# Kernel optimization log

Hardware: AMD Instinct MI355X
Metric: run time of the kernel (lower is better)

Reference implementation:

```python
import jax, jax.numpy as jnp
import numpy as np

B, D, C = 512, 512, 85742   # batch, in_features, out_features (MS1M identities)
M = 4                       # angular margin order -> cos(4*theta) = 8c^4 - 8c^2 + 1
PI = 3.14159265             # constant used in the torch source
LAMB = max(5.0, 1000.0 * (1.0 + 0.12 * 1) ** -1.0)  # lamb at iter=1 (first forward)
EPS = 1e-12                 # torch F.normalize eps


def setup_inputs() -> dict:
    key = jax.random.key(0)
    k1, k2, k3 = jax.random.split(key, 3)
    x = jax.random.normal(k1, (B, D), dtype=jnp.float32)
    label = jax.random.randint(k2, (B,), 0, C)
    limit = np.sqrt(6.0 / (D + C))  # xavier_uniform bound for weight [C, D]
    weight = jax.random.uniform(k3, (C, D), minval=-limit, maxval=limit, dtype=jnp.float32)
    return {"x": x, "weight": weight, "label": label}


def reference(x, weight, label):
    # row-normalize features and class weights (F.normalize, p=2, dim=1)
    xn = x / jnp.maximum(jnp.linalg.norm(x, axis=1, keepdims=True), EPS)
    wn = weight / jnp.maximum(jnp.linalg.norm(weight, axis=1, keepdims=True), EPS)
    cos = jnp.clip(xn @ wn.T, -1.0, 1.0)                       # [B, C] cosine logits
    cos_m = 8.0 * cos**4 - 8.0 * cos**2 + 1.0                  # cos(4*theta), m=4
    # theta/k computed on detached cos (torch uses cos_theta.data)
    theta = jnp.arccos(jax.lax.stop_gradient(cos))
    k = jnp.floor(M * theta / PI)
    phi = (-1.0) ** k * cos_m - 2.0 * k                        # [B, C]
    feat_norm = jnp.linalg.norm(x, axis=1)                     # [B]
    one_hot = jax.nn.one_hot(label, C, dtype=cos.dtype)        # scatter of 1s at label
    out = (one_hot * (phi - cos) / (1.0 + LAMB) + cos) * feat_norm[:, None]
    # cross-entropy, mean reduction
    logp = jax.nn.log_softmax(out, axis=1)
    loss = -jnp.take_along_axis(logp, label[:, None], axis=1).mean()
    return loss
```

## Files before the change

### kernel.cpp

```cpp
#include <hip/hip_runtime.h>
#include <stdint.h>

#define D_K 512
#define B_ROWS 512
#define C_CLS 85742
#define N_TILES 670
#define N_PART (N_TILES * 2)

using bf16x8 = __attribute__((ext_vector_type(8))) short;
using f32x4  = __attribute__((ext_vector_type(4))) float;

__device__ __forceinline__ unsigned short f2bf(float f) {
  unsigned int u = __builtin_bit_cast(unsigned int, f);
  u += 0x7FFFu + ((u >> 16) & 1u);
  return (unsigned short)(u >> 16);
}
__device__ __forceinline__ float bf2f(unsigned short h) {
  return __builtin_bit_cast(float, ((unsigned int)h) << 16);
}
__device__ __forceinline__ float sq8(const float4& a, const float4& b) {
  return a.x*a.x + a.y*a.y + a.z*a.z + a.w*a.w +
         b.x*b.x + b.y*b.y + b.z*b.z + b.w*b.w;
}
__device__ __forceinline__ void pack8(const float4& a, const float4& b, unsigned short* h) {
  h[0]=f2bf(a.x); h[1]=f2bf(a.y); h[2]=f2bf(a.z); h[3]=f2bf(a.w);
  h[4]=f2bf(b.x); h[5]=f2bf(b.y); h[6]=f2bf(b.z); h[7]=f2bf(b.w);
}

__global__ __launch_bounds__(256) void k_xnorm(const float* __restrict__ X,
                                               unsigned short* __restrict__ XN,
                                               float* __restrict__ FN) {
  int row  = blockIdx.x * 4 + (threadIdx.x >> 6);
  int lane = threadIdx.x & 63;
  const float4* px = (const float4*)(X + (size_t)row * D_K + lane * 8);
  float4 u = px[0], v = px[1];
  float nsq = sq8(u, v);
#pragma unroll
  for (int m = 1; m <= 32; m <<= 1) nsq += __shfl_xor(nsq, m);
  float nrm = sqrtf(nsq);
  float inv = 1.0f / fmaxf(nrm, 1e-12f);
  float4 a = make_float4(u.x*inv, u.y*inv, u.z*inv, u.w*inv);
  float4 b = make_float4(v.x*inv, v.y*inv, v.z*inv, v.w*inv);
  alignas(16) unsigned short h[8];
  pack8(a, b, h);
  *(bf16x8*)(XN + (size_t)row * D_K + lane * 8) = *(const bf16x8*)h;
  if (lane == 0) FN[row] = nrm;
}

__global__ __launch_bounds__(256) void k_gemm_lse(const float* __restrict__ W,
                                                  const unsigned short* __restrict__ XN,
                                                  const float* __restrict__ FN,
                                                  float2* __restrict__ PART) {
  __shared__ alignas(16) unsigned short As[128 * 32];
  __shared__ alignas(16) unsigned short Bs[128 * 32];
  __shared__ float nsqS[128];
  __shared__ float fnS[128];

  int bid = blockIdx.x;
  int wg    = (bid & 7) * 335 + (bid >> 3);
  int ntile = wg >> 2, mtile = wg & 3;
  int m0 = mtile * 128, n0 = ntile * 128;

  int t    = threadIdx.x;
  int lane = t & 63, wid = t >> 6;
  int wm = wid >> 1, wn = wid & 1;
  int s = lane & 15, g = lane >> 4;

  int r1 = t >> 2;
  int c0 = (t & 3) * 8;
  int gr1 = n0 + r1, gr2 = n0 + 64 + r1;
  bool v1 = gr1 < C_CLS, v2 = gr2 < C_CLS;
  const float* pB1 = W + (size_t)gr1 * D_K + c0;
  const float* pB2 = W + (size_t)gr2 * D_K + c0;

  int lin0 = wid * 512 + lane * 8;
  int lin1 = 2048 + lin0;
  const unsigned short* gA0 = XN + (size_t)(m0 + (lin0 >> 5)) * D_K + (lin0 & 31);
  const unsigned short* gA1 = XN + (size_t)(m0 + (lin1 >> 5)) * D_K + (lin1 & 31);
  unsigned short* ldsA0 = As + wid * 512;
  unsigned short* ldsA1 = As + 2048 + wid * 512;

  f32x4 acc[4][4] = {};
  float nsq1 = 0.f, nsq2 = 0.f;

  float4 ra0, ra1, rb0, rb1;
  float4 z4 = make_float4(0.f, 0.f, 0.f, 0.f);
  if (v1) { ra0 = *(const float4*)pB1; ra1 = *(const float4*)(pB1 + 4); } else { ra0 = z4; ra1 = z4; }
  if (v2) { rb0 = *(const float4*)pB2; rb1 = *(const float4*)(pB2 + 4); } else { rb0 = z4; rb1 = z4; }

  for (int kt = 0; kt < 16; ++kt) {
    __syncthreads();
    nsq1 += sq8(ra0, ra1);
    nsq2 += sq8(rb0, rb1);
    alignas(16) unsigned short h1[8], h2[8];
    pack8(ra0, ra1, h1);
    pack8(rb0, rb1, h2);
    *(bf16x8*)(Bs + t * 8)        = *(const bf16x8*)h1;
    *(bf16x8*)(Bs + 2048 + t * 8) = *(const bf16x8*)h2;
    __builtin_amdgcn_global_load_lds(
        (const __attribute__((address_space(1))) unsigned int*)(gA0 + kt * 32),
        (__attribute__((address_space(3))) unsigned int*)ldsA0, 16, 0, 0);
    __builtin_amdgcn_global_load_lds(
        (const __attribute__((address_space(1))) unsigned int*)(gA1 + kt * 32),
        (__attribute__((address_space(3))) unsigned int*)ldsA1, 16, 0, 0);
    __syncthreads();
    if (kt + 1 < 16) {
      const float* q1 = pB1 + (kt + 1) * 32;
      const float* q2 = pB2 + (kt + 1) * 32;
      if (v1) { ra0 = *(const float4*)q1; ra1 = *(const float4*)(q1 + 4); }
      if (v2) { rb0 = *(const float4*)q2; rb1 = *(const float4*)(q2 + 4); }
    }
    bf16x8 af[4], bfr[4];
#pragma unroll
    for (int mf = 0; mf < 4; ++mf)
      af[mf] = *(const bf16x8*)(As + (wm * 64 + mf * 16 + s) * 32 + g * 8);
#pragma unroll
    for (int nf = 0; nf < 4; ++nf)
      bfr[nf] = *(const bf16x8*)(Bs + (wn * 64 + nf * 16 + s) * 32 + g * 8);
#pragma unroll
    for (int mf = 0; mf < 4; ++mf)
#pragma unroll
      for (int nf = 0; nf < 4; ++nf)
        acc[mf][nf] = __builtin_amdgcn_mfma_f32_16x16x32_bf16(af[mf], bfr[nf], acc[mf][nf], 0, 0, 0);
  }

  nsq1 += __shfl_xor(nsq1, 1); nsq1 += __shfl_xor(nsq1, 2);
  nsq2 += __shfl_xor(nsq2, 1); nsq2 += __shfl_xor(nsq2, 2);
  if ((t & 3) == 0) { nsqS[r1] = nsq1; nsqS[64 + r1] = nsq2; }
  if (t < 128) fnS[t] = FN[m0 + t];
  __syncthreads();

  float rinv[4]; int cvalid[4];
#pragma unroll
  for (int nf = 0; nf < 4; ++nf) {
    int cl = wn * 64 + nf * 16 + s;
    cvalid[nf] = (n0 + cl) < C_CLS;
    rinv[nf] = 1.0f / fmaxf(sqrtf(nsqS[cl]), 1e-12f);
  }
  const float NEG_INF = -__builtin_inff();
#pragma unroll
  for (int mf = 0; mf < 4; ++mf) {
#pragma unroll
    for (int q = 0; q < 4; ++q) {
      int rl = wm * 64 + mf * 16 + g * 4 + q;
      float fr = fnS[rl];
      float z[4]; float mx = NEG_INF;
#pragma unroll
      for (int nf = 0; nf < 4; ++nf) {
        float cc = acc[mf][nf][q] * rinv[nf];
        cc = fminf(fmaxf(cc, -1.0f), 1.0f);
        z[nf] = cvalid[nf] ? cc * fr : NEG_INF;
        mx = fmaxf(mx, z[nf]);
      }
#pragma unroll
      for (int d = 1; d <= 8; d <<= 1) mx = fmaxf(mx, __shfl_xor(mx, d));
      float se = 0.f;
#pragma unroll
      for (int nf = 0; nf < 4; ++nf) se += __expf(z[nf] - mx);
#pragma unroll
      for (int d = 1; d <= 8; d <<= 1) se += __shfl_xor(se, d);
      if (s == mf * 4 + q)
        PART[(size_t)(m0 + rl) * N_PART + (ntile * 2 + wn)] = make_float2(mx, se);
    }
  }
}

__global__ __launch_bounds__(64) void k_target(const float* __restrict__ W,
                                               const unsigned short* __restrict__ XN,
                                               const float* __restrict__ FN,
                                               const int* __restrict__ LBL,
                                               float2* __restrict__ ZT) {
  int row = blockIdx.x;
  int lane = threadIdx.x;
  int lab = LBL[row];
  const float* pw = W + (size_t)lab * D_K + lane * 8;
  const unsigned short* px = XN + (size_t)row * D_K + lane * 8;
  float dot = 0.f, nsq = 0.f;
#pragma unroll
  for (int j = 0; j < 8; ++j) {
    float w = pw[j];
    nsq += w * w;
    dot += bf2f(px[j]) * bf2f(f2bf(w));
  }
#pragma unroll
  for (int m = 1; m <= 32; m <<= 1) { dot += __shfl_xor(dot, m); nsq += __shfl_xor(nsq, m); }
  if (lane == 0) {
    const float LAMB = 1000.0f / 1.12f;
    float rinv = 1.0f / fmaxf(sqrtf(nsq), 1e-12f);
    float c = fminf(fmaxf(dot * rinv, -1.0f), 1.0f);
    float c2 = c * c;
    float cm = 8.0f * c2 * c2 - 8.0f * c2 + 1.0f;
    float th = acosf(c);
    float kf = floorf(4.0f * th / 3.14159265f);
    float phi = ((((int)kf) & 1) ? -cm : cm) - 2.0f * kf;
    float fr = FN[row];
    float zu = fr * c;
    float zm = fr * (c + (phi - c) / (1.0f + LAMB));
    ZT[row] = make_float2(zu, zm);
  }
}

__global__ __launch_bounds__(256) void k_lse(const float2* __restrict__ PART,
                                             const float2* __restrict__ ZT,
                                             float* __restrict__ LOSSI) {
  int row = blockIdx.x;
  int t = threadIdx.x;
  const float NEG_INF = -__builtin_inff();
  float m = NEG_INF, ss = 0.f;
  for (int p = t; p < N_PART; p += 256) {
    float2 ps = PART[(size_t)row * N_PART + p];
    if (ps.y > 0.f) {
      if (ps.x > m) { ss = ss * __expf(m - ps.x) + ps.y; m = ps.x; }
      else          { ss += ps.y * __expf(ps.x - m); }
    }
  }
  __shared__ float sm[256], sv[256];
  sm[t] = m; sv[t] = ss;
  __syncthreads();
  for (int o = 128; o > 0; o >>= 1) {
    if (t < o) {
      float m1 = sm[t], s1 = sv[t];
      float m2 = sm[t + o], s2 = sv[t + o];
      float mm = fmaxf(m1, m2);
      float e1 = (m1 > NEG_INF) ? s1 * __expf(m1 - mm) : 0.f;
      float e2 = (m2 > NEG_INF) ? s2 * __expf(m2 - mm) : 0.f;
      sm[t] = mm; sv[t] = e1 + e2;
    }
    __syncthreads();
  }
  if (t == 0) {
    float M = sm[0], S = sv[0];
    float2 zt = ZT[row];
    S += __expf(zt.y - M) - __expf(zt.x - M);
    LOSSI[row] = M + logf(S) - zt.y;
  }
}

__global__ __launch_bounds__(256) void k_mean(const float* __restrict__ LOSSI,
                                              float* __restrict__ OUT) {
  int t = threadIdx.x;
  float s_ = LOSSI[t] + LOSSI[t + 256];
#pragma unroll
  for (int m = 1; m <= 32; m <<= 1) s_ += __shfl_xor(s_, m);
  __shared__ float wsum[4];
  if ((t & 63) == 0) wsum[t >> 6] = s_;
  __syncthreads();
  if (t == 0) OUT[0] = (wsum[0] + wsum[1] + wsum[2] + wsum[3]) * (1.0f / 512.0f);
}

extern "C" void kernel_launch(void* const* d_in, const int* in_sizes, int n_in,
                              void* d_out, int out_size, void* d_ws, size_t ws_size,
                              hipStream_t stream) {
  const float* X   = (const float*)d_in[0];
  const float* W   = (const float*)d_in[1];
  const int*   LBL = (const int*)d_in[2];
  float* OUT = (float*)d_out;

  char* ws = (char*)d_ws;
  unsigned short* XN = (unsigned short*)ws;
  float*  FN    = (float*)(ws + 524288);
  float2* ZT    = (float2*)(ws + 526336);
  float*  LOSSI = (float*)(ws + 530432);
  float2* PART  = (float2*)(ws + 532480);

  k_xnorm  <<<dim3(128),  dim3(256), 0, stream>>>(X, XN, FN);
  k_gemm_lse<<<dim3(2680), dim3(256), 0, stream>>>(W, XN, FN, PART);
  k_target <<<dim3(512),  dim3(64),  0, stream>>>(W, XN, FN, LBL, ZT);
  k_lse    <<<dim3(512),  dim3(256), 0, stream>>>(PART, ZT, LOSSI);
  k_mean   <<<dim3(1),    dim3(256), 0, stream>>>(LOSSI, OUT);
}
```

Baseline: 111.7 us.

## Double-buffer LDS tiles in GEMM with explicit waitcnt barriers

Restructures the GEMM main loop to ping-pong between two LDS buffers for both the X (bf16, loaded with async global-to-LDS copies) and W tiles. Compute on one buffer now overlaps staging of the next, and each k-step needs only one barrier with a partial vmcnt wait instead of two full syncthreads. The W load mapping also changes: each thread loads 16 contiguous floats of one row, with clamped row indices instead of zero-fill branches. The cost is double the LDS footprint and reliance on hand-written waitcnt counts matching the number of outstanding loads.

Result: slower. 145.7 us (+30.4%).

```diff
diff --git a/kernel.cpp b/kernel.cpp
--- a/kernel.cpp
+++ b/kernel.cpp
@@ -2,7 +2,6 @@
 #include <stdint.h>
 
 #define D_K 512
-#define B_ROWS 512
 #define C_CLS 85742
 #define N_TILES 670
 #define N_PART (N_TILES * 2)
@@ -51,8 +50,8 @@
                                                   const unsigned short* __restrict__ XN,
                                                   const float* __restrict__ FN,
                                                   float2* __restrict__ PART) {
-  __shared__ alignas(16) unsigned short As[128 * 32];
-  __shared__ alignas(16) unsigned short Bs[128 * 32];
+  __shared__ alignas(16) unsigned short As[2][4096];
+  __shared__ alignas(16) unsigned short Bs[2][4096];
   __shared__ float nsqS[128];
   __shared__ float fnS[128];
 
@@ -66,67 +65,87 @@
   int wm = wid >> 1, wn = wid & 1;
   int s = lane & 15, g = lane >> 4;
 
-  int r1 = t >> 2;
-  int c0 = (t & 3) * 8;
-  int gr1 = n0 + r1, gr2 = n0 + 64 + r1;
-  bool v1 = gr1 < C_CLS, v2 = gr2 < C_CLS;
-  const float* pB1 = W + (size_t)gr1 * D_K + c0;
-  const float* pB2 = W + (size_t)gr2 * D_K + c0;
-
-  int lin0 = wid * 512 + lane * 8;
-  int lin1 = 2048 + lin0;
-  const unsigned short* gA0 = XN + (size_t)(m0 + (lin0 >> 5)) * D_K + (lin0 & 31);
-  const unsigned short* gA1 = XN + (size_t)(m0 + (lin1 >> 5)) * D_K + (lin1 & 31);
-  unsigned short* ldsA0 = As + wid * 512;
-  unsigned short* ldsA1 = As + 2048 + wid * 512;
+  int gr = n0 + (t >> 1); if (gr > C_CLS - 1) gr = C_CLS - 1;
+  const float* pB = W + (size_t)gr * D_K + (t & 1) * 16;
+
+  const unsigned short* gA = XN + (size_t)(m0 + (t >> 2)) * D_K + (t & 3) * 8;
 
   f32x4 acc[4][4] = {};
-  float nsq1 = 0.f, nsq2 = 0.f;
-
-  float4 ra0, ra1, rb0, rb1;
-  float4 z4 = make_float4(0.f, 0.f, 0.f, 0.f);
-  if (v1) { ra0 = *(const float4*)pB1; ra1 = *(const float4*)(pB1 + 4); } else { ra0 = z4; ra1 = z4; }
-  if (v2) { rb0 = *(const float4*)pB2; rb1 = *(const float4*)(pB2 + 4); } else { rb0 = z4; rb1 = z4; }
-
-  for (int kt = 0; kt < 16; ++kt) {
-    __syncthreads();
-    nsq1 += sq8(ra0, ra1);
-    nsq2 += sq8(rb0, rb1);
-    alignas(16) unsigned short h1[8], h2[8];
-    pack8(ra0, ra1, h1);
-    pack8(rb0, rb1, h2);
-    *(bf16x8*)(Bs + t * 8)        = *(const bf16x8*)h1;
-    *(bf16x8*)(Bs + 2048 + t * 8) = *(const bf16x8*)h2;
-    __builtin_amdgcn_global_load_lds(
-        (const __attribute__((address_space(1))) unsigned int*)(gA0 + kt * 32),
-        (__attribute__((address_space(3))) unsigned int*)ldsA0, 16, 0, 0);
-    __builtin_amdgcn_global_load_lds(
-        (const __attribute__((address_space(1))) unsigned int*)(gA1 + kt * 32),
-        (__attribute__((address_space(3))) unsigned int*)ldsA1, 16, 0, 0);
-    __syncthreads();
-    if (kt + 1 < 16) {
-      const float* q1 = pB1 + (kt + 1) * 32;
-      const float* q2 = pB2 + (kt + 1) * 32;
-      if (v1) { ra0 = *(const float4*)q1; ra1 = *(const float4*)(q1 + 4); }
-      if (v2) { rb0 = *(const float4*)q2; rb1 = *(const float4*)(q2 + 4); }
-    }
-    bf16x8 af[4], bfr[4];
-#pragma unroll
-    for (int mf = 0; mf < 4; ++mf)
-      af[mf] = *(const bf16x8*)(As + (wm * 64 + mf * 16 + s) * 32 + g * 8);
-#pragma unroll
-    for (int nf = 0; nf < 4; ++nf)
-      bfr[nf] = *(const bf16x8*)(Bs + (wn * 64 + nf * 16 + s) * 32 + g * 8);
-#pragma unroll
-    for (int mf = 0; mf < 4; ++mf)
-#pragma unroll
-      for (int nf = 0; nf < 4; ++nf)
-        acc[mf][nf] = __builtin_amdgcn_mfma_f32_16x16x32_bf16(af[mf], bfr[nf], acc[mf][nf], 0, 0, 0);
-  }
-
-  nsq1 += __shfl_xor(nsq1, 1); nsq1 += __shfl_xor(nsq1, 2);
-  nsq2 += __shfl_xor(nsq2, 1); nsq2 += __shfl_xor(nsq2, 2);
-  if ((t & 3) == 0) { nsqS[r1] = nsq1; nsqS[64 + r1] = nsq2; }
+  float nsq = 0.f;
+  float4 rb0, rb1, rb2, rb3;
+
+#define GLDS(srcp, dstp) __builtin_amdgcn_global_load_lds( \
+    (const __attribute__((address_space(1))) unsigned int*)(srcp), \
+    (__attribute__((address_space(3))) unsigned int*)(dstp), 16, 0, 0)
+
+#define STAGE_A(b, kk) do { \
+    GLDS(gA + (size_t)(kk) * 32,             &As[b][wid * 512]); \
+    GLDS(gA + 64 * D_K + (size_t)(kk) * 32,  &As[b][2048 + wid * 512]); \
+    __builtin_amdgcn_sched_barrier(0); \
+  } while (0)
+
+#define PREF_B(kk) do { \
+    const float* q_ = pB + (kk) * 32; \
+    rb0 = *(const float4*)q_;       rb1 = *(const float4*)(q_ + 4); \
+    rb2 = *(const float4*)(q_ + 8); rb3 = *(const float4*)(q_ + 12); \
+  } while (0)
+
+#define CONV_B(b) do { \
+    nsq += sq8(rb0, rb1) + sq8(rb2, rb3); \
+    alignas(16) unsigned short h0_[8], h1_[8]; \
+    pack8(rb0, rb1, h0_); pack8(rb2, rb3, h1_); \
+    *(bf16x8*)(&Bs[b][(t >> 1) * 32 + (t & 1) * 16])     = *(const bf16x8*)h0_; \
+    *(bf16x8*)(&Bs[b][(t >> 1) * 32 + (t & 1) * 16 + 8]) = *(const bf16x8*)h1_; \
+  } while (0)
+
+#define FRAGS_MFMA(b) do { \
+    bf16x8 af[4], bfr[4]; \
+    _Pragma("unroll") for (int mf = 0; mf < 4; ++mf) \
+      af[mf] = *(const bf16x8*)(&As[b][(wm * 64 + mf * 16 + s) * 32 + g * 8]); \
+    _Pragma("unroll") for (int nf = 0; nf < 4; ++nf) \
+      bfr[nf] = *(const bf16x8*)(&Bs[b][(wn * 64 + nf * 16 + s) * 32 + g * 8]); \
+    _Pragma("unroll") for (int mf = 0; mf < 4; ++mf) \
+      _Pragma("unroll") for (int nf = 0; nf < 4; ++nf) \
+        acc[mf][nf] = __builtin_amdgcn_mfma_f32_16x16x32_bf16(af[mf], bfr[nf], acc[mf][nf], 0, 0, 0); \
+  } while (0)
+
+#define BARC() do { \
+    asm volatile("s_waitcnt vmcnt(4) lgkmcnt(0)" ::: "memory"); \
+    __builtin_amdgcn_s_barrier(); \
+    __builtin_amdgcn_sched_barrier(0); \
+  } while (0)
+#define BAR0() do { \
+    asm volatile("s_waitcnt vmcnt(0) lgkmcnt(0)" ::: "memory"); \
+    __builtin_amdgcn_s_barrier(); \
+    __builtin_amdgcn_sched_barrier(0); \
+  } while (0)
+
+  PREF_B(0);
+  STAGE_A(0, 0);
+  CONV_B(0);
+  PREF_B(1);
+  BARC();
+
+  for (int kt = 0; kt < 14; kt += 2) {
+    STAGE_A(1, kt + 1);
+    CONV_B(1);
+    PREF_B(kt + 2);
+    FRAGS_MFMA(0);
+    BARC();
+    STAGE_A(0, kt + 2);
+    CONV_B(0);
+    PREF_B(kt + 3);
+    FRAGS_MFMA(1);
+    BARC();
+  }
+  STAGE_A(1, 15);
+  CONV_B(1);
+  FRAGS_MFMA(0);
+  BAR0();
+  FRAGS_MFMA(1);
+
+  nsq += __shfl_xor(nsq, 1);
+  if ((t & 1) == 0) nsqS[t >> 1] = nsq;
   if (t < 128) fnS[t] = FN[m0 + t];
   __syncthreads();
 
```
